# Performance work log

Measured on AMD Instinct MI355X. Metric: run time of the kernel, lower is better.

## Reference

```python
import jax, jax.numpy as jnp
import numpy as np

# ---- static config (matches init_kwargs / input_specs) ----
B, GP, C, H, A = 8, 1024, 384, 6, 48          # batch, points (G-1), dim, heads, adapter dim
M = 1024                                       # number of 3D clusters
NS = 6                                         # number of 1D projection scales
GRID = 192                                     # 1D grid cells per batch element
N = B * GP                                     # total flattened points
SCALE_FACTOR = 0.5                             # args.scale_factor
COEF_PRO = 0.3                                 # args.coef_pro
EPS_LN, EPS_BN, EPS_COS = 1e-5, 1e-5, 1e-8


def setup_inputs() -> dict:
    key = jax.random.key(0)
    ks = jax.random.split(key, 10)
    rng = np.random.default_rng(0)
    # cluster assignment per point; CSR ordering = stable argsort by cluster
    cluster = rng.integers(0, M, size=N)
    order = np.argsort(cluster, kind='stable')
    seg_id = cluster[order]                    # segment id of feat[sorted_cluster_indices]
    flat_grid_index = rng.integers(0, B * GRID, size=(NS, N))
    p = lambda i, shape, s=0.02: jax.random.normal(ks[i], shape, jnp.float32) * s
    return {
        'x': jax.random.normal(ks[0], (B, GP + 1, C), jnp.float32),
        'mask': jnp.ones((NS, N, 1), jnp.float32),
        'ln1_g': jnp.ones((C,), jnp.float32), 'ln1_b': jnp.zeros((C,), jnp.float32),
        'ln2_g': jnp.ones((C,), jnp.float32), 'ln2_b': jnp.zeros((C,), jnp.float32),
        'w_in': p(1, (3 * C, C)), 'b_in': jnp.zeros((3 * C,), jnp.float32),
        'w_out': p(2, (C, C)), 'b_out': jnp.zeros((C,), jnp.float32),
        'w_fc': p(3, (4 * C, C)), 'b_fc': jnp.zeros((4 * C,), jnp.float32),
        'w_proj': p(4, (C, 4 * C)), 'b_proj': jnp.zeros((C,), jnp.float32),
        'wa1': p(5, (A, C)), 'ba1': jnp.zeros((A,), jnp.float32),
        'wa2': p(6, (C, A)), 'ba2': jnp.zeros((C,), jnp.float32),
        'g3': jnp.ones((C,), jnp.float32), 'b3': jnp.zeros((C,), jnp.float32),
        'g1d': jnp.ones((NS, C), jnp.float32), 'b1d': jnp.zeros((NS, C), jnp.float32),
        'gn3': jnp.ones((NS, C), jnp.float32), 'bn3': jnp.zeros((NS, C), jnp.float32),
        'w_attn1': p(7, (NS, C, C)), 'b_attn1': jnp.zeros((NS, C), jnp.float32),
        'sorted_cluster_indices': jnp.asarray(order, jnp.int32),
        'seg_id': jnp.asarray(seg_id, jnp.int32),
        'cluster': jnp.asarray(cluster, jnp.int32),
        'flat_grid_index': jnp.asarray(flat_grid_index, jnp.int32),
    }


def layernorm(x, g, b):
    m = x.mean(-1, keepdims=True)
    v = jnp.mean((x - m) ** 2, -1, keepdims=True)
    return (x - m) * jax.lax.rsqrt(v + EPS_LN) * g + b


def quick_gelu(x):
    return x * jax.nn.sigmoid(1.702 * x)


def bn_gelu(x, g, b):
    # BatchNorm1d (training-mode batch stats, biased var) + exact GELU
    m = x.mean(0)
    v = jnp.mean((x - m) ** 2, 0)
    y = (x - m) * jax.lax.rsqrt(v + EPS_BN) * g + b
    return jax.nn.gelu(y, approximate=False)


def seg_max_mean(x, seg, nseg):
    # fused gather-reduce: per-segment max and mean; empty segments -> 0 (torch_scatter convention)
    cnt = jax.ops.segment_sum(jnp.ones((x.shape[0],), x.dtype), seg, nseg)
    s = jax.ops.segment_sum(x, seg, nseg)
    mx = jax.ops.segment_max(x, seg, nseg)
    mx = jnp.where((cnt > 0)[:, None], mx, 0.0)
    mean = s / jnp.maximum(cnt, 1.0)[:, None]
    return mx, mean


def mha(x, w_in, b_in, w_out, b_out):
    b, g, c = x.shape
    dh = c // H
    q, k, v = jnp.split(x @ w_in.T + b_in, 3, axis=-1)
    q = q.reshape(b, g, H, dh)
    k = k.reshape(b, g, H, dh)
    v = v.reshape(b, g, H, dh)
    attn = jax.nn.softmax(jnp.einsum('bqhd,bkhd->bhqk', q, k) * (dh ** -0.5), axis=-1)
    o = jnp.einsum('bhqk,bkhd->bqhd', attn, v).reshape(b, g, c)
    return o @ w_out.T + b_out


def reference(x, mask, ln1_g, ln1_b, ln2_g, ln2_b, w_in, b_in, w_out, b_out,
              w_fc, b_fc, w_proj, b_proj, wa1, ba1, wa2, ba2, g3, b3,
              g1d, b1d, gn3, bn3, w_attn1, b_attn1,
              sorted_cluster_indices, seg_id, cluster, flat_grid_index):
    # attention + MLP + scaled adapter residual
    x = x + mha(layernorm(x, ln1_g, ln1_b), w_in, b_in, w_out, b_out)
    x_ffn = quick_gelu(layernorm(x, ln2_g, ln2_b) @ w_fc.T + b_fc) @ w_proj.T + b_proj
    adapter = quick_gelu(x_ffn @ wa1.T + ba1) @ wa2.T + ba2
    x = x + x_ffn + SCALE_FACTOR * adapter

    cls_x = x[:, :1]
    xp = x[:, 1:]                                   # [B, GP, C]
    feat = xp.reshape(-1, C)                        # [N, C]

    # 3D branch: segment_csr max/mean over clusters, BN+GELU, broadcast back
    fg = feat[sorted_cluster_indices]
    mx, mn = seg_max_mean(fg, seg_id, M)
    x_3d = bn_gelu(mx + mn, g3, b3)[cluster].reshape(B, GP, C)

    # six 1D branches: norm + projection residual, scatter max/mean to grid cells, BN+GELU, gather back
    d2_list = []
    for i in range(NS):
        y = layernorm(feat, gn3[i], bn3[i])
        y = (y @ w_attn1[i].T + b_attn1[i]) * mask[i]
        fx = y + feat
        mx1, mn1 = seg_max_mean(fx, flat_grid_index[i], B * GRID)
        d2 = bn_gelu(mx1 + mn1, g1d[i], b1d[i])[flat_grid_index[i]].reshape(B, GP, C)
        d2_list.append(d2)
    x_sup = jnp.stack(d2_list, 0)                   # [NS, B, GP, C]

    # cosine-similarity weighted fusion against the 3D branch
    def cos(a, b):
        na = jnp.maximum(jnp.linalg.norm(a, axis=-1), EPS_COS)
        nb = jnp.maximum(jnp.linalg.norm(b, axis=-1), EPS_COS)
        return jnp.sum(a * b, -1) / (na * nb)
    sims = (jax.vmap(lambda t: cos(t, x_3d))(x_sup) + 1.0) * 0.5   # [NS, B, GP]
    sims = sims / sims.sum(0, keepdims=True)
    x_sup_w = jnp.einsum('sbgc,sbg->bgc', x_sup, sims)

    xp = xp + COEF_PRO * x_sup_w
    return jnp.concatenate([cls_x, xp], axis=1)
```

## Files before the change

kernel.cpp:

```cpp
#include <hip/hip_runtime.h>
#include <hip/hip_bf16.h>
#include <float.h>
#include <math.h>

#define NB 8
#define CCH 384
#define NHEAD 6
#define DHEAD 64
#define AAD 48
#define MSEG 1024
#define NSUP 6
#define NTOK 8200
#define NFEAT 8192
#define SEG2 1536
#define SEQ 1025
#define SEQP 1088

typedef __hip_bfloat16 bf16;
typedef __attribute__((ext_vector_type(8))) short short8;
typedef __attribute__((ext_vector_type(4))) float floatx4;

static __device__ __forceinline__ long long tokrow(int n) {
  return (long long)n + (n >> 10) + 1;
}

template<int NT>
static __device__ __forceinline__ float block_reduce_sum(float v, float* s) {
  #pragma unroll
  for (int off = 32; off > 0; off >>= 1) v += __shfl_down(v, off, 64);
  int lane = threadIdx.x & 63, wid = threadIdx.x >> 6;
  if (lane == 0) s[wid] = v;
  __syncthreads();
  if (threadIdx.x == 0) {
    float t = s[0];
    #pragma unroll
    for (int w = 1; w < NT / 64; w++) t += s[w];
    s[0] = t;
  }
  __syncthreads();
  float r = s[0];
  __syncthreads();
  return r;
}

static __device__ __forceinline__ void async_copy16(void* lds, const void* g) {
  __builtin_amdgcn_global_load_lds(
      (const __attribute__((address_space(1))) unsigned int*)g,
      (__attribute__((address_space(3))) unsigned int*)lds, 16, 0, 0);
}

template<int WM, int WN>
__global__ __launch_bounds__(256) void mgemm_kernel(
    const bf16* __restrict__ A, int lda, long long sAh,
    const bf16* __restrict__ B, int ldb, long long sBh,
    float* __restrict__ outF, int ldcF, long long sCFh,
    bf16* __restrict__ outB, int ldcB, long long sCBh,
    int M, int N, int K,
    const float* __restrict__ bias, long long sBias, int act, float scale,
    const float* __restrict__ rowmask, long long sMask,
    const float* __restrict__ res1, int ldr1, int res1skip,
    const float* __restrict__ res2, int ldr2)
{
  constexpr int BM = WM * 64, BN = WN * 64;
  __shared__ uint4 Asg[BM * 8];
  __shared__ uint4 Bsg[BN * 8];
  const int z = blockIdx.z;
  const bf16* Ap = A + (long long)z * sAh;
  const bf16* Bp = B + (long long)z * sBh;
  const int tid = threadIdx.x;
  const int m0 = blockIdx.y * BM, n0 = blockIdx.x * BN;
  const int lane = tid & 63, wid = tid >> 6;
  const int wm = (wid % WM) * 64, wn = (wid / WM) * 64;
  const int q = lane >> 4, ln = lane & 15;
  const uint4 zero4 = make_uint4(0, 0, 0, 0);

  const bool fastK = ((K & 63) == 0);
  const bool fastA = fastK && (m0 + BM <= M);
  const bool fastB = fastK && (n0 + BN <= N);

  floatx4 acc[4][4];
  #pragma unroll
  for (int i = 0; i < 4; i++)
    #pragma unroll
    for (int j = 0; j < 4; j++) acc[i][j] = (floatx4){0.f, 0.f, 0.f, 0.f};

  const int nk = (K + 63) >> 6;
  for (int t = 0; t < nk; t++) {
    const int k0 = t * 64;
    __syncthreads();
    if (fastA) {
      #pragma unroll
      for (int p = 0; p < 2 * WM; p++) {
        int idx = p * 256 + tid;
        int row = idx >> 3, g = idx & 7;
        int gs = g ^ (row & 7);
        async_copy16(&Asg[p * 256 + wid * 64],
                     Ap + (long long)(m0 + row) * lda + k0 + gs * 8);
      }
    } else {
      #pragma unroll
      for (int p = 0; p < 2 * WM; p++) {
        int idx = p * 256 + tid;
        int row = idx >> 3, g = idx & 7;
        int gs = g ^ (row & 7);
        int gm = m0 + row, gk = k0 + gs * 8;
        uint4 v = zero4;
        if (gm < M && gk < K)
          v = *reinterpret_cast<const uint4*>(Ap + (long long)gm * lda + gk);
        Asg[idx] = v;
      }
    }
    if (fastB) {
      #pragma unroll
      for (int p = 0; p < 2 * WN; p++) {
        int idx = p * 256 + tid;
        int row = idx >> 3, g = idx & 7;
        int gs = g ^ (row & 7);
        async_copy16(&Bsg[p * 256 + wid * 64],
                     Bp + (long long)(n0 + row) * ldb + k0 + gs * 8);
      }
    } else {
      #pragma unroll
      for (int p = 0; p < 2 * WN; p++) {
        int idx = p * 256 + tid;
        int row = idx >> 3, g = idx & 7;
        int gs = g ^ (row & 7);
        int gn = n0 + row, gk = k0 + gs * 8;
        uint4 v = zero4;
        if (gn < N && gk < K)
          v = *reinterpret_cast<const uint4*>(Bp + (long long)gn * ldb + gk);
        Bsg[idx] = v;
      }
    }
    asm volatile("s_waitcnt vmcnt(0)" ::: "memory");
    __syncthreads();
    #pragma unroll
    for (int ks = 0; ks < 2; ks++) {
      short8 af[4], bfr[4];
      #pragma unroll
      for (int i = 0; i < 4; i++) {
        int row = wm + i * 16 + ln;
        af[i] = *reinterpret_cast<const short8*>(
            &Asg[row * 8 + ((ks * 4 + q) ^ (ln & 7))]);
      }
      #pragma unroll
      for (int j = 0; j < 4; j++) {
        int row = wn + j * 16 + ln;
        bfr[j] = *reinterpret_cast<const short8*>(
            &Bsg[row * 8 + ((ks * 4 + q) ^ (ln & 7))]);
      }
      #pragma unroll
      for (int i = 0; i < 4; i++)
        #pragma unroll
        for (int j = 0; j < 4; j++)
          acc[i][j] = __builtin_amdgcn_mfma_f32_16x16x32_bf16(af[i], bfr[j], acc[i][j], 0, 0, 0);
    }
  }

  const float* biasz = bias ? bias + z * sBias : nullptr;
  const float* rmz = rowmask ? rowmask + z * sMask : nullptr;
  float* cF = outF ? outF + (long long)z * sCFh : nullptr;
  bf16*  cB = outB ? outB + (long long)z * sCBh : nullptr;
  #pragma unroll
  for (int i = 0; i < 4; i++) {
    #pragma unroll
    for (int r = 0; r < 4; r++) {
      int gm = m0 + wm + i * 16 + q * 4 + r;
      if (gm >= M) continue;
      float rm = rmz ? rmz[gm] : 1.0f;
      long long r1off = 0;
      if (res1) r1off = (res1skip ? tokrow(gm) : (long long)gm) * ldr1;
      #pragma unroll
      for (int j = 0; j < 4; j++) {
        int gn = n0 + wn + j * 16 + ln;
        if (gn >= N) continue;
        float v = acc[i][j][r];
        if (biasz) v += biasz[gn];
        if (act) v = v / (1.0f + __expf(-1.702f * v));
        v *= scale * rm;
        if (res1) v += res1[r1off + gn];
        if (res2) v += res2[(long long)gm * ldr2 + gn];
        if (cF) cF[(long long)gm * ldcF + gn] = v;
        if (cB) cB[(long long)gm * ldcB + gn] = __float2bfloat16(v);
      }
    }
  }
}

__global__ void prep_kernel(
    const float* __restrict__ w_in, const float* __restrict__ ln1_g, bf16* __restrict__ w_in_b,
    const float* __restrict__ w_fc, const float* __restrict__ ln2_g, bf16* __restrict__ w_fc_b,
    const float* __restrict__ w_attn1, const float* __restrict__ gn3, bf16* __restrict__ wat_b,
    const float* __restrict__ w_out, bf16* __restrict__ w_out_b,
    const float* __restrict__ w_proj, bf16* __restrict__ w_pj_b,
    const float* __restrict__ wa1, bf16* __restrict__ wa1_b,
    const float* __restrict__ wa2, bf16* __restrict__ wa2_b)
{
  int y = blockIdx.y;
  int i = (blockIdx.x * 256 + threadIdx.x) * 4;
  if (y == 11) {
    if (i >= CCH * 64) return;
    int r = i >> 6, c = i & 63;
    #pragma unroll
    for (int e = 0; e < 4; e++)
      wa2_b[i + e] = __float2bfloat16((c + e) < AAD ? wa2[r * AAD + c + e] : 0.f);
    return;
  }
  const float* s; bf16* d; const float* g = nullptr; int n;
  if (y == 0)      { s = w_in;  d = w_in_b;  g = ln1_g; n = 3 * CCH * CCH; }
  else if (y == 1) { s = w_fc;  d = w_fc_b;  g = ln2_g; n = 4 * CCH * CCH; }
  else if (y <= 7) { int z = y - 2;
                     s = w_attn1 + (long long)z * CCH * CCH;
                     d = wat_b   + (long long)z * CCH * CCH;
                     g = gn3 + z * CCH; n = CCH * CCH; }
  else if (y == 8) { s = w_out;  d = w_out_b; n = CCH * CCH; }
  else if (y == 9) { s = w_proj; d = w_pj_b;  n = 4 * CCH * CCH; }
  else             { s = wa1;   d = wa1_b;   n = AAD * CCH; }
  if (i >= n) return;
  float4 v = *reinterpret_cast<const float4*>(s + i);
  if (g) {
    int k = i % CCH;
    v.x *= g[k]; v.y *= g[k + 1]; v.z *= g[k + 2]; v.w *= g[k + 3];
  }
  d[i]     = __float2bfloat16(v.x);
  d[i + 1] = __float2bfloat16(v.y);
  d[i + 2] = __float2bfloat16(v.z);
  d[i + 3] = __float2bfloat16(v.w);
}

__global__ __launch_bounds__(64) void fold_kernel(
    const float* __restrict__ w_in, const float* __restrict__ b_in,
    const float* __restrict__ ln1_b, float* __restrict__ b_in_f,
    const float* __restrict__ w_fc, const float* __restrict__ b_fc,
    const float* __restrict__ ln2_b, float* __restrict__ b_fc_f,
    const float* __restrict__ w_attn1, const float* __restrict__ b_attn1,
    const float* __restrict__ bn3, float* __restrict__ b_at_f)
{
  int y = blockIdx.y, n = blockIdx.x;
  const float* W; const float* b; const float* beta; float* o; int rows;
  if (y == 0)      { W = w_in; b = b_in; beta = ln1_b; o = b_in_f; rows = 3 * CCH; }
  else if (y == 1) { W = w_fc; b = b_fc; beta = ln2_b; o = b_fc_f; rows = 4 * CCH; }
  else             { int z = y - 2;
                     W = w_attn1 + (long long)z * CCH * CCH; b = b_attn1 + z * CCH;
                     beta = bn3 + z * CCH; o = b_at_f + z * CCH; rows = CCH; }
  if (n >= rows) return;
  const float* Wr = W + (long long)n * CCH;
  float s = 0.f;
  for (int k = threadIdx.x; k < CCH; k += 64) s += Wr[k] * beta[k];
  #pragma unroll
  for (int off = 32; off > 0; off >>= 1) s += __shfl_down(s, off, 64);
  if (threadIdx.x == 0) o[n] = b[n] + s;
}

__global__ __launch_bounds__(256) void norm_kernel(
    const float* __restrict__ in, bf16* __restrict__ out, int skipcls, int nrows)
{
  int r = blockIdx.x * 4 + (threadIdx.x >> 6);
  if (r >= nrows) return;
  int lane = threadIdx.x & 63;
  long long ir = skipcls ? tokrow(r) : (long long)r;
  const float* x = in + ir * CCH;
  float v[6];
  float s = 0.f, s2 = 0.f;
  #pragma unroll
  for (int k = 0; k < 6; k++) {
    v[k] = x[lane + k * 64];
    s += v[k]; s2 += v[k] * v[k];
  }
  #pragma unroll
  for (int off = 32; off > 0; off >>= 1) {
    s  += __shfl_xor(s, off, 64);
    s2 += __shfl_xor(s2, off, 64);
  }
  float m = s * (1.0f / CCH);
  float var = s2 * (1.0f / CCH) - m * m;
  float rstd = rsqrtf(var + 1e-5f);
  bf16* o = out + (long long)r * CCH;
  #pragma unroll
  for (int k = 0; k < 6; k++)
    o[lane + k * 64] = __float2bfloat16((v[k] - m) * rstd);
}

__global__ __launch_bounds__(256) void vtrans_kernel(
    const bf16* __restrict__ qkv, bf16* __restrict__ Vt)
{
  __shared__ bf16 tile[64][68];
  int bh = blockIdx.y;
  int b = bh / NHEAD, h = bh % NHEAD;
  int s0 = blockIdx.x * 64;
  int dq = (threadIdx.x & 15) * 4;
  int sl = threadIdx.x >> 4;
  #pragma unroll
  for (int p = 0; p < 4; p++) {
    int sloc = sl + p * 16;
    int s = s0 + sloc;
    uint2 v = make_uint2(0, 0);
    if (s < SEQ)
      v = *reinterpret_cast<const uint2*>(
            qkv + ((long long)(b * SEQ + s)) * (3 * CCH) + 2 * CCH + h * DHEAD + dq);
    *reinterpret_cast<uint2*>(&tile[sloc][dq]) = v;
  }
  __syncthreads();
  #pragma unroll
  for (int p = 0; p < 4; p++) {
    int dloc = sl + p * 16;
    int s4 = dq;
    bf16 t0 = tile[s4 + 0][dloc], t1 = tile[s4 + 1][dloc];
    bf16 t2 = tile[s4 + 2][dloc], t3 = tile[s4 + 3][dloc];
    bf16* dst = Vt + ((long long)bh * DHEAD + dloc) * SEQP + s0 + s4;
    dst[0] = t0; dst[1] = t1; dst[2] = t2; dst[3] = t3;
  }
}

__global__ __launch_bounds__(256) void flash_kernel(
    const bf16* __restrict__ qkv, const bf16* __restrict__ Vt,
    bf16* __restrict__ O)
{
  __shared__ uint4 Kt[64 * 9];
  __shared__ uint4 Vtt[64 * 9];
  __shared__ uint4 Pt[64 * 9];
  const int bh = blockIdx.y;
  const int b = bh / NHEAD, h = bh % NHEAD;
  const int q0 = blockIdx.x * 64;
  const int tid = threadIdx.x;
  const int lane = tid & 63, w = tid >> 6;
  const int q = lane >> 4, ln = lane & 15;
  const uint4 zero4 = make_uint4(0, 0, 0, 0);

  short8 aq[2];
  {
    int qrow = q0 + w * 16 + ln;
    #pragma unroll
    for (int ks = 0; ks < 2; ks++) {
      if (qrow < SEQ)
        aq[ks] = *reinterpret_cast<const short8*>(
            qkv + ((long long)(b * SEQ + qrow)) * (3 * CCH) + h * DHEAD + ks * 32 + q * 8);
      else
        aq[ks] = (short8){0, 0, 0, 0, 0, 0, 0, 0};
    }
  }

  floatx4 oacc[4];
  #pragma unroll
  for (int j = 0; j < 4; j++) oacc[j] = (floatx4){0.f, 0.f, 0.f, 0.f};
  float m_i[4], l_i[4];
  #pragma unroll
  for (int r = 0; r < 4; r++) { m_i[r] = -FLT_MAX; l_i[r] = 0.f; }

  for (int kt = 0; kt < SEQP / 64; kt++) {
    __syncthreads();
    #pragma unroll
    for (int p = 0; p < 2; p++) {
      int g = p * 256 + tid;
      int row = g >> 3, k8 = g & 7;
      int sg = kt * 64 + row;
      uint4 kv = zero4;
      if (sg < SEQ)
        kv = *reinterpret_cast<const uint4*>(
              qkv + ((long long)(b * SEQ + sg)) * (3 * CCH) + CCH + h * DHEAD + k8 * 8);
      Kt[row * 9 + k8] = kv;
      Vtt[row * 9 + k8] = *reinterpret_cast<const uint4*>(
              Vt + ((long long)bh * DHEAD + row) * SEQP + kt * 64 + k8 * 8);
    }
    __syncthreads();

    floatx4 sa[4];
    #pragma unroll
    for (int j = 0; j < 4; j++) sa[j] = (floatx4){0.f, 0.f, 0.f, 0.f};
    #pragma unroll
    for (int ks = 0; ks < 2; ks++) {
      #pragma unroll
      for (int j = 0; j < 4; j++) {
        short8 kb = *reinterpret_cast<const short8*>(&Kt[(j * 16 + ln) * 9 + ks * 4 + q]);
        sa[j] = __builtin_amdgcn_mfma_f32_16x16x32_bf16(aq[ks], kb, sa[j], 0, 0, 0);
      }
    }

    bf16* pbase = reinterpret_cast<bf16*>(Pt);
    #pragma unroll
    for (int r = 0; r < 4; r++) {
      float mx = -FLT_MAX;
      #pragma unroll
      for (int j = 0; j < 4; j++) {
        float s = sa[j][r] * 0.125f;
        int key = kt * 64 + j * 16 + ln;
        s = (key < SEQ) ? s : -FLT_MAX;
        sa[j][r] = s;
        mx = fmaxf(mx, s);
      }
      #pragma unroll
      for (int off = 1; off < 16; off <<= 1) mx = fmaxf(mx, __shfl_xor(mx, off, 16));
      float mnew = fmaxf(m_i[r], mx);
      float alpha = __expf(m_i[r] - mnew);
      m_i[r] = mnew;
      float rs = 0.f;
      #pragma unroll
      for (int j = 0; j < 4; j++) {
        float p = __expf(sa[j][r] - mnew);
        sa[j][r] = p;
        rs += p;
      }
      #pragma unroll
      for (int off = 1; off < 16; off <<= 1) rs += __shfl_xor(rs, off, 16);
      l_i[r] = l_i[r] * alpha + rs;
      #pragma unroll
      for (int j = 0; j < 4; j++) oacc[j][r] *= alpha;
      bf16* prow = pbase + (w * 16 + q * 4 + r) * 72;
      #pragma unroll
      for (int j = 0; j < 4; j++) prow[j * 16 + ln] = __float2bfloat16(sa[j][r]);
    }
    #pragma unroll
    for (int ks = 0; ks < 2; ks++) {
      short8 ap = *reinterpret_cast<const short8*>(pbase + (w * 16 + ln) * 72 + ks * 32 + q * 8);
      #pragma unroll
      for (int j = 0; j < 4; j++) {
        short8 vb = *reinterpret_cast<const short8*>(&Vtt[(j * 16 + ln) * 9 + ks * 4 + q]);
        oacc[j] = __builtin_amdgcn_mfma_f32_16x16x32_bf16(ap, vb, oacc[j], 0, 0, 0);
      }
    }
  }

  #pragma unroll
  for (int r = 0; r < 4; r++) {
    int qrow = q0 + w * 16 + q * 4 + r;
    if (qrow >= SEQ) continue;
    float inv = 1.0f / l_i[r];
    bf16* orow = O + ((long long)(b * SEQ + qrow)) * CCH + h * DHEAD;
    #pragma unroll
    for (int j = 0; j < 4; j++)
      orow[j * 16 + ln] = __float2bfloat16(oacc[j][r] * inv);
  }
}

__global__ __launch_bounds__(128) void seg1_kernel(
    const float* __restrict__ x2, const int* __restrict__ sorted_idx,
    const int* __restrict__ seg_id, float* __restrict__ s3)
{
  int s = blockIdx.x;
  int lo = 0, hi = NFEAT;
  while (lo < hi) { int mid = (lo + hi) >> 1; if (seg_id[mid] < s) lo = mid + 1; else hi = mid; }
  int start = lo;
  hi = NFEAT;
  while (lo < hi) { int mid = (lo + hi) >> 1; if (seg_id[mid] < s + 1) lo = mid + 1; else hi = mid; }
  int end = lo;
  int cnt = end - start;
  for (int c = threadIdx.x; c < CCH; c += 128) {
    float sum = 0.f, mx = -FLT_MAX;
    for (int r = start; r < end; r++) {
      int n = sorted_idx[r];
      float v = x2[tokrow(n) * CCH + c];
      sum += v; mx = fmaxf(mx, v);
    }
    float u = (cnt > 0 ? mx : 0.f) + sum / fmaxf((float)cnt, 1.0f);
    s3[(long long)s * CCH + c] = u;
  }
}

__global__ void hist0_kernel(int* __restrict__ cnt)
{
  int idx = blockIdx.x * 256 + threadIdx.x;
  if (idx < NSUP * SEG2) cnt[idx] = 0;
}
__global__ void hist_kernel(const int* __restrict__ fgi, int* __restrict__ cnt)
{
  int idx = blockIdx.x * 256 + threadIdx.x;
  if (idx >= NSUP * NFEAT) return;
  int z = idx >> 13;
  atomicAdd(&cnt[z * SEG2 + fgi[idx]], 1);
}
__global__ __launch_bounds__(256) void scan_kernel(
    const int* __restrict__ cnt, int* __restrict__ base, int* __restrict__ cur)
{
  int z = blockIdx.x, t = threadIdx.x;
  __shared__ int sdata[256];
  const int* c = cnt + z * SEG2;
  int loc[6]; int s = 0;
  #pragma unroll
  for (int e = 0; e < 6; e++) { loc[e] = s; s += c[t * 6 + e]; }
  sdata[t] = s;
  __syncthreads();
  for (int off = 1; off < 256; off <<= 1) {
    int v = (t >= off) ? sdata[t - off] : 0;
    __syncthreads();
    sdata[t] += v;
    __syncthreads();
  }
  int pre = (t > 0) ? sdata[t - 1] : 0;
  #pragma unroll
  for (int e = 0; e < 6; e++) {
    int b = pre + loc[e];
    base[z * SEG2 + t * 6 + e] = b;
    cur[z * SEG2 + t * 6 + e] = b;
  }
}
__global__ void place_kernel(const int* __restrict__ fgi, int* __restrict__ cur,
                             int* __restrict__ order)
{
  int idx = blockIdx.x * 256 + threadIdx.x;
  if (idx >= NSUP * NFEAT) return;
  int z = idx >> 13, n = idx & (NFEAT - 1);
  int s = fgi[idx];
  int pos = atomicAdd(&cur[z * SEG2 + s], 1);
  order[z * NFEAT + pos] = n;
}

__global__ __launch_bounds__(128) void seg2_kernel(
    const bf16* __restrict__ fx, const int* __restrict__ base,
    const int* __restrict__ cnt, const int* __restrict__ order,
    float* __restrict__ u)
{
  int s = blockIdx.x, z = blockIdx.y;
  int st = base[z * SEG2 + s], c = cnt[z * SEG2 + s];
  const int* ord = order + z * NFEAT;
  const bf16* fz = fx + (long long)z * NFEAT * CCH;
  for (int ch = threadIdx.x; ch < CCH; ch += 128) {
    float sum = 0.f, mx = -FLT_MAX;
    for (int r = 0; r < c; r++) {
      float v = __bfloat162float(fz[(long long)ord[st + r] * CCH + ch]);
      sum += v; mx = fmaxf(mx, v);
    }
    u[((long long)z * SEG2 + s) * CCH + ch] = (c > 0 ? mx : 0.f) + sum / fmaxf((float)c, 1.0f);
  }
}

__global__ __launch_bounds__(256) void bnstats_kernel(
    const float* __restrict__ u, long long sU, int rows,
    float* __restrict__ mean, float* __restrict__ var, long long sMV)
{
  int c = blockIdx.x, z = blockIdx.y;
  u += z * sU; mean += z * sMV; var += z * sMV;
  float s = 0.f, s2 = 0.f;
  for (int r = threadIdx.x; r < rows; r += 256) {
    float v = u[(long long)r * CCH + c];
    s += v; s2 += v * v;
  }
  __shared__ float sb[4];
  s  = block_reduce_sum<256>(s, sb);
  s2 = block_reduce_sum<256>(s2, sb);
  if (threadIdx.x == 0) {
    float m = s / rows;
    mean[c] = m;
    var[c] = s2 / rows - m * m;
  }
}

__global__ __launch_bounds__(128) void bnapply_kernel(
    const float* __restrict__ u, long long sU,
    const float* __restrict__ mean, const float* __restrict__ var, long long sMV,
    const float* __restrict__ g, const float* __restrict__ b, long long sGB,
    float* __restrict__ t, long long sT, float* __restrict__ norms, long long sN)
{
  int r = blockIdx.x, z = blockIdx.y;
  u += z * sU; mean += z * sMV; var += z * sMV; g += z * sGB; b += z * sGB;
  t += z * sT; norms += z * sN;
  float ss = 0.f;
  #pragma unroll
  for (int e = 0; e < 3; e++) {
    int c = threadIdx.x + e * 128;
    float v = u[(long long)r * CCH + c];
    float y = (v - mean[c]) * rsqrtf(var[c] + 1e-5f) * g[c] + b[c];
    float ge = 0.5f * y * (1.0f + erff(y * 0.70710678118654752f));
    t[(long long)r * CCH + c] = ge;
    ss += ge * ge;
  }
  __shared__ float sb[2];
  ss = block_reduce_sum<128>(ss, sb);
  if (threadIdx.x == 0) norms[r] = sqrtf(ss);
}

__global__ __launch_bounds__(256) void final_kernel(
    const float* __restrict__ x2, const float* __restrict__ t3,
    const float* __restrict__ t3norm, const float* __restrict__ t1d,
    const float* __restrict__ t1dnorm, const int* __restrict__ cluster,
    const int* __restrict__ fgi, float* __restrict__ out)
{
  int row = blockIdx.x * 4 + (threadIdx.x >> 6);
  if (row >= NTOK) return;
  int lane = threadIdx.x & 63;
  int b = row / SEQ, gg = row - b * SEQ;
  const float* xr = x2 + (long long)row * CCH;
  float* orow = out + (long long)row * CCH;
  float xv[6];
  #pragma unroll
  for (int k = 0; k < 6; k++) xv[k] = xr[lane + k * 64];
  if (gg == 0) {
    #pragma unroll
    for (int k = 0; k < 6; k++) orow[lane + k * 64] = xv[k];
    return;
  }
  int n = b * 1024 + gg - 1;
  int c3 = cluster[n];
  const float* a3 = t3 + (long long)c3 * CCH;
  float a3v[6];
  #pragma unroll
  for (int k = 0; k < 6; k++) a3v[k] = a3[lane + k * 64];
  float nb = fmaxf(t3norm[c3], 1e-8f);
  float w[NSUP];
  const float* rows[NSUP];
  float tot = 0.f;
  #pragma unroll
  for (int i = 0; i < NSUP; i++) {
    int s = fgi[i * NFEAT + n];
    const float* ar = t1d + ((long long)i * SEG2 + s) * CCH;
    rows[i] = ar;
    float d = 0.f;
    #pragma unroll
    for (int k = 0; k < 6; k++) d += ar[lane + k * 64] * a3v[k];
    #pragma unroll
    for (int off = 32; off > 0; off >>= 1) d += __shfl_xor(d, off, 64);
    float na = fmaxf(t1dnorm[i * SEG2 + s], 1e-8f);
    float cosv = d / (na * nb);
    w[i] = (cosv + 1.0f) * 0.5f;
    tot += w[i];
  }
  float inv = 1.0f / tot;
  #pragma unroll
  for (int k = 0; k < 6; k++) {
    float acc = 0.f;
    #pragma unroll
    for (int i = 0; i < NSUP; i++) acc += w[i] * rows[i][lane + k * 64];
    orow[lane + k * 64] = xv[k] + 0.3f * acc * inv;
  }
}

extern "C" void kernel_launch(void* const* d_in, const int* in_sizes, int n_in,
                              void* d_out, int out_size, void* d_ws, size_t ws_size,
                              hipStream_t stream)
{
  const float* x_in   = (const float*)d_in[0];
  const float* maskp  = (const float*)d_in[1];
  const float* ln1_g  = (const float*)d_in[2];
  const float* ln1_b  = (const float*)d_in[3];
  const float* ln2_g  = (const float*)d_in[4];
  const float* ln2_b  = (const float*)d_in[5];
  const float* w_in   = (const float*)d_in[6];
  const float* b_in   = (const float*)d_in[7];
  const float* w_out  = (const float*)d_in[8];
  const float* b_out  = (const float*)d_in[9];
  const float* w_fc   = (const float*)d_in[10];
  const float* b_fc   = (const float*)d_in[11];
  const float* w_proj = (const float*)d_in[12];
  const float* b_proj = (const float*)d_in[13];
  const float* wa1    = (const float*)d_in[14];
  const float* ba1    = (const float*)d_in[15];
  const float* wa2    = (const float*)d_in[16];
  const float* ba2    = (const float*)d_in[17];
  const float* g3     = (const float*)d_in[18];
  const float* b3     = (const float*)d_in[19];
  const float* g1d    = (const float*)d_in[20];
  const float* b1d    = (const float*)d_in[21];
  const float* gn3    = (const float*)d_in[22];
  const float* bn3    = (const float*)d_in[23];
  const float* w_attn1= (const float*)d_in[24];
  const float* b_attn1= (const float*)d_in[25];
  const int* sorted_idx = (const int*)d_in[26];
  const int* seg_id   = (const int*)d_in[27];
  const int* cluster  = (const int*)d_in[28];
  const int* fgi      = (const int*)d_in[29];
  float* out = (float*)d_out;
  char* wsb = (char*)d_ws;

  size_t off = 0;
  auto alloc = [&](size_t bytes) { size_t o = off; off += (bytes + 255) & ~(size_t)255; return o; };
  size_t o_qkv  = alloc((size_t)NTOK * 3 * CCH * 2);
  size_t o_Vt   = alloc((size_t)NB * NHEAD * DHEAD * SEQP * 2);
  size_t o_hbf  = alloc((size_t)NTOK * CCH * 2);
  size_t o_obf  = alloc((size_t)NTOK * CCH * 2);
  size_t o_x1   = alloc((size_t)NTOK * CCH * 4);
  size_t o_x2   = alloc((size_t)NTOK * CCH * 4);
  size_t o_ffn  = alloc((size_t)NTOK * CCH * 4);
  size_t o_tbf  = alloc((size_t)NTOK * 64 * 2);
  size_t o_fx   = alloc((size_t)NSUP * NFEAT * CCH * 2);
  size_t o_s3   = alloc((size_t)MSEG * CCH * 4);
  size_t o_t3   = alloc((size_t)MSEG * CCH * 4);
  size_t o_t3n  = alloc((size_t)MSEG * 4);
  size_t o_mean = alloc((size_t)NSUP * CCH * 4);
  size_t o_var  = alloc((size_t)NSUP * CCH * 4);
  size_t o_ssum = alloc((size_t)NSUP * SEG2 * CCH * 4);
  size_t o_t1d  = alloc((size_t)NSUP * SEG2 * CCH * 4);
  size_t o_t1dn = alloc((size_t)NSUP * SEG2 * 4);
  size_t o_cnt  = alloc((size_t)NSUP * SEG2 * 4);
  size_t o_base = alloc((size_t)NSUP * SEG2 * 4);
  size_t o_cur  = alloc((size_t)NSUP * SEG2 * 4);
  size_t o_ord  = alloc((size_t)NSUP * NFEAT * 4);
  size_t o_wib  = alloc((size_t)3 * CCH * CCH * 2);
  size_t o_wob  = alloc((size_t)CCH * CCH * 2);
  size_t o_wfb  = alloc((size_t)4 * CCH * CCH * 2);
  size_t o_wpb  = alloc((size_t)CCH * 4 * CCH * 2);
  size_t o_wa1b = alloc((size_t)AAD * CCH * 2);
  size_t o_wa2b = alloc((size_t)CCH * 64 * 2);
  size_t o_watb = alloc((size_t)NSUP * CCH * CCH * 2);
  size_t o_bib  = alloc((size_t)3 * CCH * 4);
  size_t o_bfb  = alloc((size_t)4 * CCH * 4);
  size_t o_bab  = alloc((size_t)NSUP * CCH * 4);

  bf16*  qkv_bf = (bf16*)(wsb + o_qkv);
  bf16*  Vt     = (bf16*)(wsb + o_Vt);
  bf16*  h_bf   = (bf16*)(wsb + o_hbf);
  bf16*  o_bf   = (bf16*)(wsb + o_obf);
  float* x1     = (float*)(wsb + o_x1);
  float* x2     = (float*)(wsb + o_x2);
  float* ffn    = (float*)(wsb + o_ffn);
  bf16*  t_bf   = (bf16*)(wsb + o_tbf);
  bf16*  fx     = (bf16*)(wsb + o_fx);
  float* s3     = (float*)(wsb + o_s3);
  float* t3     = (float*)(wsb + o_t3);
  float* t3n    = (float*)(wsb + o_t3n);
  float* meanb  = (float*)(wsb + o_mean);
  float* varb   = (float*)(wsb + o_var);
  float* ssum   = (float*)(wsb + o_ssum);
  float* t1d    = (float*)(wsb + o_t1d);
  float* t1dn   = (float*)(wsb + o_t1dn);
  int*   cntb   = (int*)(wsb + o_cnt);
  int*   baseb  = (int*)(wsb + o_base);
  int*   curb   = (int*)(wsb + o_cur);
  int*   ordb   = (int*)(wsb + o_ord);
  bf16*  w_in_b = (bf16*)(wsb + o_wib);
  bf16*  w_out_b= (bf16*)(wsb + o_wob);
  bf16*  w_fc_b = (bf16*)(wsb + o_wfb);
  bf16*  w_pj_b = (bf16*)(wsb + o_wpb);
  bf16*  wa1_b  = (bf16*)(wsb + o_wa1b);
  bf16*  wa2_b  = (bf16*)(wsb + o_wa2b);
  bf16*  wat_b  = (bf16*)(wsb + o_watb);
  float* b_in_f = (float*)(wsb + o_bib);
  float* b_fc_f = (float*)(wsb + o_bfb);
  float* b_at_f = (float*)(wsb + o_bab);
  bf16*  fc_bf  = (bf16*)(wsb + o_qkv);
  bf16*  ffn_bf = (bf16*)(wsb + o_obf);

  prep_kernel<<<dim3((4 * CCH * CCH / 4 + 255) / 256, 12), 256, 0, stream>>>(
      w_in, ln1_g, w_in_b, w_fc, ln2_g, w_fc_b, w_attn1, gn3, wat_b,
      w_out, w_out_b, w_proj, w_pj_b, wa1, wa1_b, wa2, wa2_b);
  fold_kernel<<<dim3(4 * CCH, 8), 64, 0, stream>>>(
      w_in, b_in, ln1_b, b_in_f, w_fc, b_fc, ln2_b, b_fc_f,
      w_attn1, b_attn1, bn3, b_at_f);
  hipMemsetAsync(t_bf, 0, (size_t)NTOK * 64 * 2, stream);
  hist0_kernel<<<(NSUP * SEG2 + 255) / 256, 256, 0, stream>>>(cntb);
  hist_kernel<<<(NSUP * NFEAT + 255) / 256, 256, 0, stream>>>(fgi, cntb);
  scan_kernel<<<NSUP, 256, 0, stream>>>(cntb, baseb, curb);
  place_kernel<<<(NSUP * NFEAT + 255) / 256, 256, 0, stream>>>(fgi, curb, ordb);

  norm_kernel<<<(NTOK + 3) / 4, 256, 0, stream>>>(x_in, h_bf, 0, NTOK);
  mgemm_kernel<2, 2><<<dim3(9, 65, 1), 256, 0, stream>>>(
      h_bf, CCH, 0, w_in_b, CCH, 0, nullptr, 0, 0, qkv_bf, 3 * CCH, 0,
      NTOK, 3 * CCH, CCH, b_in_f, 0, 0, 1.0f, nullptr, 0, nullptr, 0, 0, nullptr, 0);
  vtrans_kernel<<<dim3(SEQP / 64, NB * NHEAD), 256, 0, stream>>>(qkv_bf, Vt);
  flash_kernel<<<dim3(SEQP / 64, NB * NHEAD), 256, 0, stream>>>(qkv_bf, Vt, o_bf);
  mgemm_kernel<2, 2><<<dim3(3, 65, 1), 256, 0, stream>>>(
      o_bf, CCH, 0, w_out_b, CCH, 0, x1, CCH, 0, nullptr, 0, 0,
      NTOK, CCH, CCH, b_out, 0, 0, 1.0f, nullptr, 0, x_in, CCH, 0, nullptr, 0);
  norm_kernel<<<(NTOK + 3) / 4, 256, 0, stream>>>(x1, h_bf, 0, NTOK);
  mgemm_kernel<2, 2><<<dim3(12, 65, 1), 256, 0, stream>>>(
      h_bf, CCH, 0, w_fc_b, CCH, 0, nullptr, 0, 0, fc_bf, 4 * CCH, 0,
      NTOK, 4 * CCH, CCH, b_fc_f, 0, 1, 1.0f, nullptr, 0, nullptr, 0, 0, nullptr, 0);
  mgemm_kernel<2, 2><<<dim3(3, 65, 1), 256, 0, stream>>>(
      fc_bf, 4 * CCH, 0, w_pj_b, 4 * CCH, 0, ffn, CCH, 0, ffn_bf, CCH, 0,
      NTOK, CCH, 4 * CCH, b_proj, 0, 0, 1.0f, nullptr, 0, nullptr, 0, 0, nullptr, 0);
  mgemm_kernel<4, 1><<<dim3(1, 33, 1), 256, 0, stream>>>(
      ffn_bf, CCH, 0, wa1_b, CCH, 0, nullptr, 0, 0, t_bf, 64, 0,
      NTOK, AAD, CCH, ba1, 0, 1, 1.0f, nullptr, 0, nullptr, 0, 0, nullptr, 0);
  mgemm_kernel<2, 2><<<dim3(3, 65, 1), 256, 0, stream>>>(
      t_bf, 64, 0, wa2_b, 64, 0, x2, CCH, 0, nullptr, 0, 0,
      NTOK, CCH, 64, ba2, 0, 0, 0.5f, nullptr, 0, x1, CCH, 0, ffn, CCH);
  seg1_kernel<<<MSEG, 128, 0, stream>>>(x2, sorted_idx, seg_id, s3);
  bnstats_kernel<<<dim3(CCH, 1), 256, 0, stream>>>(s3, 0, MSEG, meanb, varb, 0);
  bnapply_kernel<<<dim3(MSEG, 1), 128, 0, stream>>>(s3, 0, meanb, varb, 0,
      g3, b3, 0, t3, 0, t3n, 0);
  norm_kernel<<<(NFEAT + 3) / 4, 256, 0, stream>>>(x2, h_bf, 1, NFEAT);
  mgemm_kernel<2, 2><<<dim3(3, 64, NSUP), 256, 0, stream>>>(
      h_bf, CCH, 0, wat_b, CCH, (long long)CCH * CCH,
      nullptr, 0, 0, fx, CCH, (long long)NFEAT * CCH,
      NFEAT, CCH, CCH, b_at_f, CCH, 0, 1.0f, maskp, NFEAT, x2, CCH, 1, nullptr, 0);
  seg2_kernel<<<dim3(SEG2, NSUP), 128, 0, stream>>>(fx, baseb, cntb, ordb, ssum);
  bnstats_kernel<<<dim3(CCH, NSUP), 256, 0, stream>>>(
      ssum, (long long)SEG2 * CCH, SEG2, meanb, varb, CCH);
  bnapply_kernel<<<dim3(SEG2, NSUP), 128, 0, stream>>>(
      ssum, (long long)SEG2 * CCH, meanb, varb, CCH,
      g1d, b1d, CCH, t1d, (long long)SEG2 * CCH, t1dn, SEG2);
  final_kernel<<<(NTOK + 3) / 4, 256, 0, stream>>>(
      x2, t3, t3n, t1d, t1dn, cluster, fgi, out);
}
```

Measured before the change: 651.6 us.

## Register-prefetch GEMM pipeline with narrower N tiles and doubled grid

The GEMM drops the async global-to-LDS copies and stages each next K-tile through registers while the MFMAs run on the current tile, then writes that tile to LDS between barriers. The N tile is halved (each wave computes 64x32), so every launch doubles its grid in x, and the adapter GEMM moves from the 4x1 config to 2x2. The goal is to hide global-load latency behind compute and to put more blocks in flight. In exchange, every block reloads the A tile for fewer output columns, and register pressure rises from the prefetch buffers.

```diff
diff --git a/kernel.cpp b/kernel.cpp
--- a/kernel.cpp
+++ b/kernel.cpp
@@ -43,12 +43,6 @@
   return r;
 }
 
-static __device__ __forceinline__ void async_copy16(void* lds, const void* g) {
-  __builtin_amdgcn_global_load_lds(
-      (const __attribute__((address_space(1))) unsigned int*)g,
-      (__attribute__((address_space(3))) unsigned int*)lds, 16, 0, 0);
-}
-
 template<int WM, int WN>
 __global__ __launch_bounds__(256) void mgemm_kernel(
     const bf16* __restrict__ A, int lda, long long sAh,
@@ -61,7 +55,7 @@
     const float* __restrict__ res1, int ldr1, int res1skip,
     const float* __restrict__ res2, int ldr2)
 {
-  constexpr int BM = WM * 64, BN = WN * 64;
+  constexpr int BM = WM * 64, BN = WN * 32;
   __shared__ uint4 Asg[BM * 8];
   __shared__ uint4 Bsg[BN * 8];
   const int z = blockIdx.z;
@@ -70,73 +64,54 @@
   const int tid = threadIdx.x;
   const int m0 = blockIdx.y * BM, n0 = blockIdx.x * BN;
   const int lane = tid & 63, wid = tid >> 6;
-  const int wm = (wid % WM) * 64, wn = (wid / WM) * 64;
+  const int wm = (wid % WM) * 64, wn = (wid / WM) * 32;
   const int q = lane >> 4, ln = lane & 15;
   const uint4 zero4 = make_uint4(0, 0, 0, 0);
 
-  const bool fastK = ((K & 63) == 0);
-  const bool fastA = fastK && (m0 + BM <= M);
-  const bool fastB = fastK && (n0 + BN <= N);
-
-  floatx4 acc[4][4];
+  uint4 areg[2 * WM], breg[WN];
+
+  auto loadregs = [&](int k0) {
+    #pragma unroll
+    for (int p = 0; p < 2 * WM; p++) {
+      int idx = p * 256 + tid;
+      int row = idx >> 3, g = idx & 7;
+      int gs = g ^ (row & 7);
+      int gm = m0 + row, gk = k0 + gs * 8;
+      areg[p] = (gm < M && gk < K)
+          ? *reinterpret_cast<const uint4*>(Ap + (long long)gm * lda + gk) : zero4;
+    }
+    #pragma unroll
+    for (int p = 0; p < WN; p++) {
+      int idx = p * 256 + tid;
+      int row = idx >> 3, g = idx & 7;
+      int gs = g ^ (row & 7);
+      int gn = n0 + row, gk = k0 + gs * 8;
+      breg[p] = (gn < N && gk < K)
+          ? *reinterpret_cast<const uint4*>(Bp + (long long)gn * ldb + gk) : zero4;
+    }
+  };
+  auto writeLDS = [&]() {
+    #pragma unroll
+    for (int p = 0; p < 2 * WM; p++) Asg[p * 256 + tid] = areg[p];
+    #pragma unroll
+    for (int p = 0; p < WN; p++) Bsg[p * 256 + tid] = breg[p];
+  };
+
+  floatx4 acc[4][2];
   #pragma unroll
   for (int i = 0; i < 4; i++)
     #pragma unroll
-    for (int j = 0; j < 4; j++) acc[i][j] = (floatx4){0.f, 0.f, 0.f, 0.f};
+    for (int j = 0; j < 2; j++) acc[i][j] = (floatx4){0.f, 0.f, 0.f, 0.f};
 
   const int nk = (K + 63) >> 6;
+  loadregs(0);
+  writeLDS();
+  __syncthreads();
   for (int t = 0; t < nk; t++) {
-    const int k0 = t * 64;
-    __syncthreads();
-    if (fastA) {
-      #pragma unroll
-      for (int p = 0; p < 2 * WM; p++) {
-        int idx = p * 256 + tid;
-        int row = idx >> 3, g = idx & 7;
-        int gs = g ^ (row & 7);
-        async_copy16(&Asg[p * 256 + wid * 64],
-                     Ap + (long long)(m0 + row) * lda + k0 + gs * 8);
-      }
-    } else {
-      #pragma unroll
-      for (int p = 0; p < 2 * WM; p++) {
-        int idx = p * 256 + tid;
-        int row = idx >> 3, g = idx & 7;
-        int gs = g ^ (row & 7);
-        int gm = m0 + row, gk = k0 + gs * 8;
-        uint4 v = zero4;
-        if (gm < M && gk < K)
-          v = *reinterpret_cast<const uint4*>(Ap + (long long)gm * lda + gk);
-        Asg[idx] = v;
-      }
-    }
-    if (fastB) {
-      #pragma unroll
-      for (int p = 0; p < 2 * WN; p++) {
-        int idx = p * 256 + tid;
-        int row = idx >> 3, g = idx & 7;
-        int gs = g ^ (row & 7);
-        async_copy16(&Bsg[p * 256 + wid * 64],
-                     Bp + (long long)(n0 + row) * ldb + k0 + gs * 8);
-      }
-    } else {
-      #pragma unroll
-      for (int p = 0; p < 2 * WN; p++) {
-        int idx = p * 256 + tid;
-        int row = idx >> 3, g = idx & 7;
-        int gs = g ^ (row & 7);
-        int gn = n0 + row, gk = k0 + gs * 8;
-        uint4 v = zero4;
-        if (gn < N && gk < K)
-          v = *reinterpret_cast<const uint4*>(Bp + (long long)gn * ldb + gk);
-        Bsg[idx] = v;
-      }
-    }
-    asm volatile("s_waitcnt vmcnt(0)" ::: "memory");
-    __syncthreads();
+    if (t + 1 < nk) loadregs((t + 1) * 64);
     #pragma unroll
     for (int ks = 0; ks < 2; ks++) {
-      short8 af[4], bfr[4];
+      short8 af[4], bfr[2];
       #pragma unroll
       for (int i = 0; i < 4; i++) {
         int row = wm + i * 16 + ln;
@@ -144,7 +119,7 @@
             &Asg[row * 8 + ((ks * 4 + q) ^ (ln & 7))]);
       }
       #pragma unroll
-      for (int j = 0; j < 4; j++) {
+      for (int j = 0; j < 2; j++) {
         int row = wn + j * 16 + ln;
         bfr[j] = *reinterpret_cast<const short8*>(
             &Bsg[row * 8 + ((ks * 4 + q) ^ (ln & 7))]);
@@ -152,8 +127,13 @@
       #pragma unroll
       for (int i = 0; i < 4; i++)
         #pragma unroll
-        for (int j = 0; j < 4; j++)
+        for (int j = 0; j < 2; j++)
           acc[i][j] = __builtin_amdgcn_mfma_f32_16x16x32_bf16(af[i], bfr[j], acc[i][j], 0, 0, 0);
+    }
+    if (t + 1 < nk) {
+      __syncthreads();
+      writeLDS();
+      __syncthreads();
     }
   }
 
@@ -171,7 +151,7 @@
       long long r1off = 0;
       if (res1) r1off = (res1skip ? tokrow(gm) : (long long)gm) * ldr1;
       #pragma unroll
-      for (int j = 0; j < 4; j++) {
+      for (int j = 0; j < 2; j++) {
         int gn = n0 + wn + j * 16 + ln;
         if (gn >= N) continue;
         float v = acc[i][j][r];
@@ -741,25 +721,25 @@
   place_kernel<<<(NSUP * NFEAT + 255) / 256, 256, 0, stream>>>(fgi, curb, ordb);
 
   norm_kernel<<<(NTOK + 3) / 4, 256, 0, stream>>>(x_in, h_bf, 0, NTOK);
-  mgemm_kernel<2, 2><<<dim3(9, 65, 1), 256, 0, stream>>>(
+  mgemm_kernel<2, 2><<<dim3(18, 65, 1), 256, 0, stream>>>(
       h_bf, CCH, 0, w_in_b, CCH, 0, nullptr, 0, 0, qkv_bf, 3 * CCH, 0,
       NTOK, 3 * CCH, CCH, b_in_f, 0, 0, 1.0f, nullptr, 0, nullptr, 0, 0, nullptr, 0);
   vtrans_kernel<<<dim3(SEQP / 64, NB * NHEAD), 256, 0, stream>>>(qkv_bf, Vt);
   flash_kernel<<<dim3(SEQP / 64, NB * NHEAD), 256, 0, stream>>>(qkv_bf, Vt, o_bf);
-  mgemm_kernel<2, 2><<<dim3(3, 65, 1), 256, 0, stream>>>(
+  mgemm_kernel<2, 2><<<dim3(6, 65, 1), 256, 0, stream>>>(
       o_bf, CCH, 0, w_out_b, CCH, 0, x1, CCH, 0, nullptr, 0, 0,
       NTOK, CCH, CCH, b_out, 0, 0, 1.0f, nullptr, 0, x_in, CCH, 0, nullptr, 0);
   norm_kernel<<<(NTOK + 3) / 4, 256, 0, stream>>>(x1, h_bf, 0, NTOK);
-  mgemm_kernel<2, 2><<<dim3(12, 65, 1), 256, 0, stream>>>(
+  mgemm_kernel<2, 2><<<dim3(24, 65, 1), 256, 0, stream>>>(
       h_bf, CCH, 0, w_fc_b, CCH, 0, nullptr, 0, 0, fc_bf, 4 * CCH, 0,
       NTOK, 4 * CCH, CCH, b_fc_f, 0, 1, 1.0f, nullptr, 0, nullptr, 0, 0, nullptr, 0);
-  mgemm_kernel<2, 2><<<dim3(3, 65, 1), 256, 0, stream>>>(
+  mgemm_kernel<2, 2><<<dim3(6, 65, 1), 256, 0, stream>>>(
       fc_bf, 4 * CCH, 0, w_pj_b, 4 * CCH, 0, ffn, CCH, 0, ffn_bf, CCH, 0,
       NTOK, CCH, 4 * CCH, b_proj, 0, 0, 1.0f, nullptr, 0, nullptr, 0, 0, nullptr, 0);
-  mgemm_kernel<4, 1><<<dim3(1, 33, 1), 256, 0, stream>>>(
+  mgemm_kernel<2, 2><<<dim3(1, 65, 1), 256, 0, stream>>>(
       ffn_bf, CCH, 0, wa1_b, CCH, 0, nullptr, 0, 0, t_bf, 64, 0,
       NTOK, AAD, CCH, ba1, 0, 1, 1.0f, nullptr, 0, nullptr, 0, 0, nullptr, 0);
-  mgemm_kernel<2, 2><<<dim3(3, 65, 1), 256, 0, stream>>>(
+  mgemm_kernel<2, 2><<<dim3(6, 65, 1), 256, 0, stream>>>(
       t_bf, 64, 0, wa2_b, 64, 0, x2, CCH, 0, nullptr, 0, 0,
       NTOK, CCH, 64, ba2, 0, 0, 0.5f, nullptr, 0, x1, CCH, 0, ffn, CCH);
   seg1_kernel<<<MSEG, 128, 0, stream>>>(x2, sorted_idx, seg_id, s3);
@@ -767,7 +747,7 @@
   bnapply_kernel<<<dim3(MSEG, 1), 128, 0, stream>>>(s3, 0, meanb, varb, 0,
       g3, b3, 0, t3, 0, t3n, 0);
   norm_kernel<<<(NFEAT + 3) / 4, 256, 0, stream>>>(x2, h_bf, 1, NFEAT);
-  mgemm_kernel<2, 2><<<dim3(3, 64, NSUP), 256, 0, stream>>>(
+  mgemm_kernel<2, 2><<<dim3(6, 64, NSUP), 256, 0, stream>>>(
       h_bf, CCH, 0, wat_b, CCH, (long long)CCH * CCH,
       nullptr, 0, 0, fx, CCH, (long long)NFEAT * CCH,
       NFEAT, CCH, CCH, b_at_f, CCH, 0, 1.0f, maskp, NFEAT, x2, CCH, 1, nullptr, 0);
```

After: 812.4 us. 24.7% more time.
